# Kernel tuning notes

Hardware: AMD Instinct MI355X
Metric: run time of the kernel (lower is better)

Reference implementation:

```python
import jax, jax.numpy as jnp
import numpy as np

N = 100_000      # nodes
E = 1_600_000    # edges (avg degree 16)
H = 128          # hidden_channels == num_node_features
L = 6            # SAGEConv layers (third=True)
G = 128          # graphs in batch (for global_mean_pool)
C = 10           # num_classes
EPS = 1e-5       # BatchNorm eps


def setup_inputs() -> dict:
    key = jax.random.key(0)
    ks = jax.random.split(key, 8)
    s = 1.0 / np.sqrt(H)
    x = jax.random.normal(ks[0], (N, H), jnp.float32)
    edge_index = jax.random.randint(ks[1], (2, E), 0, N, dtype=jnp.int32)
    batch = jnp.sort(jax.random.randint(ks[2], (N,), 0, G, dtype=jnp.int32))
    return {
        "x": x,
        "edge_index": edge_index,
        "batch": batch,
        "Wl": jax.random.normal(ks[3], (L, H, H), jnp.float32) * s,  # neighbor lin
        "bl": jnp.zeros((L, H), jnp.float32),
        "Wr": jax.random.normal(ks[4], (L, H, H), jnp.float32) * s,  # root lin (no bias)
        "gamma": jnp.ones((L, H), jnp.float32),
        "beta": jnp.zeros((L, H), jnp.float32),
        "lin_W": jax.random.normal(ks[5], (H, C), jnp.float32) * s,
        "lin_b": jnp.zeros((C,), jnp.float32),
    }


def reference(x, edge_index, batch, Wl, bl, Wr, gamma, beta, lin_W, lin_b):
    src, dst = edge_index[0], edge_index[1]
    n = x.shape[0]
    # in-degree for mean aggregation (constant across layers)
    deg = jax.ops.segment_sum(jnp.ones((src.shape[0],), x.dtype), dst, num_segments=n)
    inv_deg = jnp.where(deg > 0, 1.0 / deg, 0.0)[:, None]  # [n,1]

    for l in range(Wl.shape[0]):
        # SAGEConv: lin_l(mean_{j->i} x_j) + lin_r(x_i)
        agg = jax.ops.segment_sum(x[src], dst, num_segments=n) * inv_deg  # [n,H]
        h = agg @ Wl[l] + bl[l] + x @ Wr[l]
        # BatchNorm1d (training-style batch stats, biased variance)
        mu = jnp.mean(h, axis=0)
        var = jnp.mean((h - mu) ** 2, axis=0)
        h = (h - mu) * jax.lax.rsqrt(var + EPS) * gamma[l] + beta[l]
        x = jax.nn.relu(h)

    # global_mean_pool over graph ids
    cnt = jax.ops.segment_sum(jnp.ones((n,), x.dtype), batch, num_segments=G)
    pooled = jax.ops.segment_sum(x, batch, num_segments=G) / jnp.maximum(cnt, 1.0)[:, None]
    # dropout(p=0.5) is identity in eval mode
    return pooled @ lin_W + lin_b  # [G, C]
```

## Files before the change

kernel.cpp:

```cpp
#include <hip/hip_runtime.h>
#include <hip/hip_bf16.h>

#define N_NODES 100000
#define N_EDGES 1600000
#define HDIM    128
#define NLAYER  6
#define NGRAPH  128
#define NCLASS  10
#define BN_EPS  1e-5f

#define POOL_SPLIT 16

#define NBUCK   196
#define BSH     9
#define KC_BLOCKS 250
#define KC_CHUNK  6400
#define LCOL_CAP  10240

#define GBM 128
#define NBLK_G ((N_NODES + GBM - 1) / GBM)

typedef __attribute__((ext_vector_type(8))) short short8v;
typedef __attribute__((ext_vector_type(4))) float f32x4;
typedef __attribute__((ext_vector_type(2))) float f32x2;
typedef __attribute__((ext_vector_type(4))) int int4v;
typedef __attribute__((ext_vector_type(2))) int int2v;

__device__ __forceinline__ float b2f(unsigned short h) {
    return __uint_as_float(((unsigned int)h) << 16);
}
__device__ __forceinline__ unsigned short f2b(float f) {
    unsigned int u = __float_as_uint(f);
    u += 0x7FFF + ((u >> 16) & 1);
    return (unsigned short)(u >> 16);
}
__device__ __forceinline__ void gl_lds16(const void* g, void* l) {
    __builtin_amdgcn_global_load_lds((const __attribute__((address_space(1))) unsigned int*)g,
                                     (__attribute__((address_space(3))) unsigned int*)l,
                                     16, 0, 0);
}
__device__ __forceinline__ short8v bn_pack(short8v v, float4 scA, float4 scB,
                                           float4 shA, float4 shB) {
    short8v o;
    o[0] = (short)f2b(fmaxf(0.f, b2f((unsigned short)v[0]) * scA.x + shA.x));
    o[1] = (short)f2b(fmaxf(0.f, b2f((unsigned short)v[1]) * scA.y + shA.y));
    o[2] = (short)f2b(fmaxf(0.f, b2f((unsigned short)v[2]) * scA.z + shA.z));
    o[3] = (short)f2b(fmaxf(0.f, b2f((unsigned short)v[3]) * scA.w + shA.w));
    o[4] = (short)f2b(fmaxf(0.f, b2f((unsigned short)v[4]) * scB.x + shB.x));
    o[5] = (short)f2b(fmaxf(0.f, b2f((unsigned short)v[5]) * scB.y + shB.y));
    o[6] = (short)f2b(fmaxf(0.f, b2f((unsigned short)v[6]) * scB.z + shB.z));
    o[7] = (short)f2b(fmaxf(0.f, b2f((unsigned short)v[7]) * scB.w + shB.w));
    return o;
}


__global__ void __launch_bounds__(256) k_hist(const int* __restrict__ dst,
                                              int* __restrict__ bcnt) {
    __shared__ int h[NBUCK];
    for (int i = threadIdx.x; i < NBUCK; i += 256) h[i] = 0;
    __syncthreads();
    const int4v* d4 = (const int4v*)dst;
    int base = blockIdx.x * (KC_CHUNK / 4);
    for (int i = threadIdx.x; i < KC_CHUNK / 4; i += 256) {
        int4v d = __builtin_nontemporal_load(d4 + base + i);
        atomicAdd(&h[d[0] >> BSH], 1);
        atomicAdd(&h[d[1] >> BSH], 1);
        atomicAdd(&h[d[2] >> BSH], 1);
        atomicAdd(&h[d[3] >> BSH], 1);
    }
    __syncthreads();
    for (int i = threadIdx.x; i < NBUCK; i += 256)
        if (h[i]) atomicAdd(&bcnt[i], h[i]);
}

__global__ void k_bscan(const int* __restrict__ bcnt, int* __restrict__ boff,
                        int* __restrict__ bcur, int* __restrict__ row_off) {
    if (threadIdx.x == 0 && blockIdx.x == 0) {
        int acc = 0;
        for (int i = 0; i < NBUCK; ++i) {
            boff[i] = acc; bcur[i] = acc; acc += bcnt[i];
        }
        boff[NBUCK] = acc;
        row_off[N_NODES] = N_EDGES;
    }
}

__global__ void __launch_bounds__(256) k_part(const int* __restrict__ src,
                                              const int* __restrict__ dst,
                                              int* __restrict__ bcur,
                                              int2v* __restrict__ P) {
    __shared__ int h[NBUCK];
    __shared__ int gbase[NBUCK];
    for (int i = threadIdx.x; i < NBUCK; i += 256) h[i] = 0;
    __syncthreads();
    const int4v* d4 = (const int4v*)dst;
    const int4v* s4 = (const int4v*)src;
    const int base = blockIdx.x * (KC_CHUNK / 4);
    for (int i = threadIdx.x; i < KC_CHUNK / 4; i += 256) {
        int4v d = __builtin_nontemporal_load(d4 + base + i);
        atomicAdd(&h[d[0] >> BSH], 1);
        atomicAdd(&h[d[1] >> BSH], 1);
        atomicAdd(&h[d[2] >> BSH], 1);
        atomicAdd(&h[d[3] >> BSH], 1);
    }
    __syncthreads();
    for (int i = threadIdx.x; i < NBUCK; i += 256) {
        int c = h[i];
        gbase[i] = c ? atomicAdd(&bcur[i], c) : 0;
        h[i] = 0;
    }
    __syncthreads();
    for (int i = threadIdx.x; i < KC_CHUNK / 4; i += 256) {
        int4v d = __builtin_nontemporal_load(d4 + base + i);
        int4v s = __builtin_nontemporal_load(s4 + base + i);
#pragma unroll
        for (int k = 0; k < 4; ++k) {
            int b = d[k] >> BSH;
            int pos = gbase[b] + atomicAdd(&h[b], 1);
            int2v pr; pr[0] = s[k]; pr[1] = d[k];
            P[pos] = pr;
        }
    }
}

__global__ void __launch_bounds__(1024) k_bucket(const int2v* __restrict__ P,
                                                 const int* __restrict__ boff,
                                                 int* __restrict__ row_off,
                                                 int* __restrict__ col) {
    __shared__ int ldeg[512];
    __shared__ int lcur[512];
    __shared__ int lcol[LCOL_CAP];
    const int tid = threadIdx.x;
    const int b = blockIdx.x;
    const int pbeg = boff[b], pend = boff[b + 1];
    const int nE = pend - pbeg;
    const int n0 = b << BSH;
    if (tid < 512) ldeg[tid] = 0;
    __syncthreads();
    for (int i = tid; i < nE; i += 1024) {
        int2v pr = P[pbeg + i];
        atomicAdd(&ldeg[pr[1] - n0], 1);
    }
    __syncthreads();
    int myd = (tid < 512) ? ldeg[tid] : 0;
    for (int off = 1; off < 512; off <<= 1) {
        int t = 0;
        if (tid < 512 && tid >= off) t = ldeg[tid - off];
        __syncthreads();
        if (tid < 512) ldeg[tid] += t;
        __syncthreads();
    }
    if (tid < 512) {
        int excl = ldeg[tid] - myd;
        lcur[tid] = excl;
        int node = n0 + tid;
        if (node < N_NODES) row_off[node] = pbeg + excl;
    }
    __syncthreads();
    for (int i = tid; i < nE; i += 1024) {
        int2v pr = P[pbeg + i];
        int pos = atomicAdd(&lcur[pr[1] - n0], 1);
        if (pos < LCOL_CAP) lcol[pos] = pr[0];
    }
    __syncthreads();
    for (int i = tid; i < nE; i += 1024) col[pbeg + i] = lcol[i];
}


__global__ void __launch_bounds__(256) k_cvt_x(const float* __restrict__ x,
                                               unsigned short* __restrict__ Xb,
                                               unsigned int* __restrict__ X8) {
    int idx = blockIdx.x * 256 + threadIdx.x;
    f32x4 v = __builtin_nontemporal_load(((const f32x4*)x) + idx);
    ushort4 o = { f2b(v[0]), f2b(v[1]), f2b(v[2]), f2b(v[3]) };
    ((ushort4*)Xb)[idx] = o;
    unsigned int d = 0;
    d = __builtin_amdgcn_cvt_pk_fp8_f32(v[0], v[1], d, false);
    d = __builtin_amdgcn_cvt_pk_fp8_f32(v[2], v[3], d, true);
    X8[idx] = d;
}

__global__ void __launch_bounds__(256) k_cvt_w(const float* __restrict__ Wl,
                                               const float* __restrict__ Wr,
                                               unsigned short* __restrict__ Wtb) {
    int idx = blockIdx.x * 256 + threadIdx.x;
    int kk = idx & 255;
    int n  = (idx >> 8) & 127;
    int l  = idx >> 15;
    float v = (kk < HDIM) ? Wl[l * HDIM * HDIM + kk * HDIM + n]
                          : Wr[l * HDIM * HDIM + (kk - HDIM) * HDIM + n];
    Wtb[idx] = f2b(v);
}

__global__ void __launch_bounds__(256) k_bnx8(const unsigned short* __restrict__ Hb,
                                              const float* __restrict__ scsh,
                                              int2v* __restrict__ X8) {
    int idx = blockIdx.x * 256 + threadIdx.x;
    int c8 = (idx & 15) * 8;
    short8v v = ((const short8v*)Hb)[idx];
    float f[8];
#pragma unroll
    for (int j = 0; j < 8; ++j)
        f[j] = fmaxf(0.f, b2f((unsigned short)v[j]) * scsh[c8 + j] + scsh[HDIM + c8 + j]);
    unsigned int d0 = 0, d1 = 0;
    d0 = __builtin_amdgcn_cvt_pk_fp8_f32(f[0], f[1], d0, false);
    d0 = __builtin_amdgcn_cvt_pk_fp8_f32(f[2], f[3], d0, true);
    d1 = __builtin_amdgcn_cvt_pk_fp8_f32(f[4], f[5], d1, false);
    d1 = __builtin_amdgcn_cvt_pk_fp8_f32(f[6], f[7], d1, true);
    int2v o; o[0] = (int)d0; o[1] = (int)d1;
    X8[idx] = o;
}


__global__ void __launch_bounds__(256) k_agg8(const unsigned char* __restrict__ X8,
                                              const int* __restrict__ row_off,
                                              const int* __restrict__ col,
                                              unsigned short* __restrict__ AGGb) {
    __shared__ int lcol[4096];
    __shared__ int sro[33];
    const int tid = threadIdx.x;
    const int nb0 = blockIdx.x * 32;
    if (tid <= 32) sro[tid] = row_off[nb0 + tid];
    __syncthreads();
    const int s0 = sro[0];
    const int nE = sro[32] - s0;
    const bool fits = (nE <= 4096);
    if (fits) {
        for (int i = tid; i < nE; i += 256) lcol[i] = col[s0 + i];
    }
    __syncthreads();

    const int g   = tid >> 3;
    const int c16 = (tid & 7) * 16;
    const int s = sro[g] - s0, e = sro[g + 1] - s0;
    const int* cp = fits ? lcol : (col + s0);

    f32x2 a2[8] = {};
    auto accum = [&](int4v v) {
#pragma unroll
        for (int q = 0; q < 4; ++q) {
            unsigned int w = (unsigned int)v[q];
            a2[2 * q]     += __builtin_amdgcn_cvt_pk_f32_fp8(w, false);
            a2[2 * q + 1] += __builtin_amdgcn_cvt_pk_f32_fp8(w, true);
        }
    };

    int p = s;
    for (; p + 8 <= e; p += 8) {
        int nbx[8];
#pragma unroll
        for (int j = 0; j < 8; ++j) nbx[j] = cp[p + j];
        int4v v[8];
#pragma unroll
        for (int j = 0; j < 8; ++j)
            v[j] = *(const int4v*)(X8 + (size_t)nbx[j] * HDIM + c16);
#pragma unroll
        for (int j = 0; j < 8; ++j) accum(v[j]);
    }
    if (p + 4 <= e) {
        int nbx[4];
#pragma unroll
        for (int j = 0; j < 4; ++j) nbx[j] = cp[p + j];
        int4v v[4];
#pragma unroll
        for (int j = 0; j < 4; ++j)
            v[j] = *(const int4v*)(X8 + (size_t)nbx[j] * HDIM + c16);
#pragma unroll
        for (int j = 0; j < 4; ++j) accum(v[j]);
        p += 4;
    }
    for (; p < e; ++p) {
        int4v v0 = *(const int4v*)(X8 + (size_t)cp[p] * HDIM + c16);
        accum(v0);
    }

    float w = (e > s) ? 1.0f / (float)(e - s) : 0.f;
    short8v o0, o1;
#pragma unroll
    for (int j = 0; j < 8; ++j) o0[j] = (short)f2b(a2[j >> 1][j & 1] * w);
#pragma unroll
    for (int j = 0; j < 8; ++j) o1[j] = (short)f2b(a2[4 + (j >> 1)][j & 1] * w);
    unsigned short* dst = AGGb + (size_t)(nb0 + g) * HDIM + c16;
    *(short8v*)dst = o0;
    *(short8v*)(dst + 8) = o1;
}


__global__ void __launch_bounds__(512) k_gemm_l0(const unsigned short* __restrict__ AGGb,
                                                 const unsigned short* __restrict__ Xb,
                                                 const unsigned short* __restrict__ Wtb,
                                                 const float* __restrict__ bl,
                                                 unsigned short* __restrict__ Hb,
                                                 float* __restrict__ pstat) {
    __shared__ __align__(16) char smem[32768];
    const int tid  = threadIdx.x;
    const int bm   = blockIdx.x * GBM;
    const int wv   = tid >> 6;
    const int lane = tid & 63;
    const int li   = lane & 15, hi = lane >> 4;
    const int wm   = wv & 1, wn = wv >> 1;

    f32x4 acc[4][2] = {};
    const int rr = tid >> 2, sk = tid & 3;
    const int swz = ((sk ^ (rr & 3)) << 4);

    auto stage = [&](int b, int step) {
        const unsigned short* Asrc = (step < 4) ? AGGb : Xb;
        const int kk0 = (step & 3) * 32;
        {
            int row = bm + rr; if (row >= N_NODES) row = N_NODES - 1;
            gl_lds16((const char*)(Asrc + (size_t)row * HDIM + kk0) + swz,
                     smem + b * 8192 + wv * 1024);
        }
        const int k0 = step * 32;
        gl_lds16((const char*)(Wtb + (size_t)rr * 256 + k0) + swz,
                 smem + 16384 + b * 8192 + wv * 1024);
    };

    stage(0, 0);
    __syncthreads();

    int buf = 0;
    for (int step = 0; step < 8; ++step) {
        if (step < 7) stage(buf ^ 1, step + 1);
        char* bA = smem + buf * 8192;
        char* bW = smem + 16384 + buf * 8192;
        short8v afr[4], bfr[2];
#pragma unroll
        for (int m = 0; m < 4; ++m) {
            int r = wm * 64 + m * 16 + li;
            afr[m] = *(const short8v*)(bA + r * 64 + ((hi ^ (r & 3)) << 4));
        }
#pragma unroll
        for (int nf = 0; nf < 2; ++nf) {
            int n = wn * 32 + nf * 16 + li;
            bfr[nf] = *(const short8v*)(bW + n * 64 + ((hi ^ (n & 3)) << 4));
        }
#pragma unroll
        for (int m = 0; m < 4; ++m)
#pragma unroll
            for (int nf = 0; nf < 2; ++nf)
                acc[m][nf] = __builtin_amdgcn_mfma_f32_16x16x32_bf16(afr[m], bfr[nf],
                                                                     acc[m][nf], 0, 0, 0);
        __syncthreads();
        buf ^= 1;
    }

    float* st = (float*)smem;
#pragma unroll
    for (int nf = 0; nf < 2; ++nf) {
        int c = wn * 32 + nf * 16 + li;
        float bb = bl[c];
        float ls = 0.f, lq = 0.f;
#pragma unroll
        for (int m = 0; m < 4; ++m) {
            int row0 = bm + wm * 64 + m * 16 + hi * 4;
#pragma unroll
            for (int j = 0; j < 4; ++j) {
                int row = row0 + j;
                if (row < N_NODES) {
                    float v = acc[m][nf][j] + bb;
                    Hb[(size_t)row * HDIM + c] = f2b(v);
                    ls += v; lq += v * v;
                }
            }
        }
        ls += __shfl_xor(ls, 16); ls += __shfl_xor(ls, 32);
        lq += __shfl_xor(lq, 16); lq += __shfl_xor(lq, 32);
        if (hi == 0) {
            st[wv * 128 + c] = ls;
            st[1024 + wv * 128 + c] = lq;
        }
    }
    __syncthreads();
    if (tid < 128) {
        int w0 = (tid >> 5) * 2;
        float s = st[w0 * 128 + tid] + st[(w0 + 1) * 128 + tid];
        pstat[blockIdx.x * 256 + tid] = s;
    } else if (tid < 256) {
        int c = tid - 128;
        int w0 = (c >> 5) * 2;
        float q = st[1024 + w0 * 128 + c] + st[1024 + (w0 + 1) * 128 + c];
        pstat[blockIdx.x * 256 + tid] = q;
    }
}

__global__ void __launch_bounds__(512) k_gemm_fuse(const unsigned short* __restrict__ AGGb,
                                                   const unsigned short* __restrict__ Hprev,
                                                   const float* __restrict__ scsh,
                                                   const unsigned short* __restrict__ Wtb,
                                                   const float* __restrict__ bl,
                                                   unsigned short* __restrict__ Hb,
                                                   float* __restrict__ pstat) {
    __shared__ __align__(16) char smem[32768];
    const int tid  = threadIdx.x;
    const int bm   = blockIdx.x * GBM;
    const int wv   = tid >> 6;
    const int lane = tid & 63;
    const int li   = lane & 15, hi = lane >> 4;
    const int wm   = wv & 1, wn = wv >> 1;

    f32x4 acc[4][2] = {};
    const int rr = tid >> 2, sk = tid & 3;
    const int swz = ((sk ^ (rr & 3)) << 4);

    auto stageW = [&](int b, int step) {
        const int k0 = step * 32;
        gl_lds16((const char*)(Wtb + (size_t)rr * 256 + k0) + swz,
                 smem + 16384 + b * 8192 + wv * 1024);
    };
    auto stageA = [&](int b, int step) {
        const int kk0 = step * 32;
        int row = bm + rr; if (row >= N_NODES) row = N_NODES - 1;
        gl_lds16((const char*)(AGGb + (size_t)row * HDIM + kk0) + swz,
                 smem + b * 8192 + wv * 1024);
    };

    stageA(0, 0); stageW(0, 0);
    __syncthreads();

    int buf = 0;
    for (int step = 0; step < 8; ++step) {
        char* curA = smem + buf * 8192;
        char* curW = smem + 16384 + buf * 8192;
        char* nxtA = smem + (buf ^ 1) * 8192;
        const int ns = step + 1;
        short8v rv;
        int c0 = 0;
        bool regstage = false;
        if (step < 7) {
            stageW(buf ^ 1, ns);
            if (ns < 4) {
                stageA(buf ^ 1, ns);
            } else {
                regstage = true;
                c0 = (ns - 4) * 32 + sk * 8;
                int row = bm + rr; if (row >= N_NODES) row = N_NODES - 1;
                rv = *(const short8v*)(Hprev + (size_t)row * HDIM + c0);
            }
        }

        short8v afr[4], bfr[2];
#pragma unroll
        for (int m = 0; m < 4; ++m) {
            int r = wm * 64 + m * 16 + li;
            afr[m] = *(const short8v*)(curA + r * 64 + ((hi ^ (r & 3)) << 4));
        }
#pragma unroll
        for (int nf = 0; nf < 2; ++nf) {
            int n = wn * 32 + nf * 16 + li;
            bfr[nf] = *(const short8v*)(curW + n * 64 + ((hi ^ (n & 3)) << 4));
        }
#pragma unroll
        for (int m = 0; m < 4; ++m)
#pragma unroll
            for (int nf = 0; nf < 2; ++nf)
                acc[m][nf] = __builtin_amdgcn_mfma_f32_16x16x32_bf16(afr[m], bfr[nf],
                                                                     acc[m][nf], 0, 0, 0);

        if (regstage) {
            float4 scA = *(const float4*)&scsh[c0];
            float4 scB = *(const float4*)&scsh[c0 + 4];
            float4 shA = *(const float4*)&scsh[HDIM + c0];
            float4 shB = *(const float4*)&scsh[HDIM + c0 + 4];
            *(short8v*)(nxtA + rr * 64 + swz) = bn_pack(rv, scA, scB, shA, shB);
        }
        __syncthreads();
        buf ^= 1;
    }

    float* st = (float*)smem;
#pragma unroll
    for (int nf = 0; nf < 2; ++nf) {
        int c = wn * 32 + nf * 16 + li;
        float bb = bl[c];
        float ls = 0.f, lq = 0.f;
#pragma unroll
        for (int m = 0; m < 4; ++m) {
            int row0 = bm + wm * 64 + m * 16 + hi * 4;
#pragma unroll
            for (int j = 0; j < 4; ++j) {
                int row = row0 + j;
                if (row < N_NODES) {
                    float v = acc[m][nf][j] + bb;
                    Hb[(size_t)row * HDIM + c] = f2b(v);
                    ls += v; lq += v * v;
                }
            }
        }
        ls += __shfl_xor(ls, 16); ls += __shfl_xor(ls, 32);
        lq += __shfl_xor(lq, 16); lq += __shfl_xor(lq, 32);
        if (hi == 0) {
            st[wv * 128 + c] = ls;
            st[1024 + wv * 128 + c] = lq;
        }
    }
    __syncthreads();
    if (tid < 128) {
        int w0 = (tid >> 5) * 2;
        float s = st[w0 * 128 + tid] + st[(w0 + 1) * 128 + tid];
        pstat[blockIdx.x * 256 + tid] = s;
    } else if (tid < 256) {
        int c = tid - 128;
        int w0 = (c >> 5) * 2;
        float q = st[1024 + w0 * 128 + c] + st[1024 + (w0 + 1) * 128 + c];
        pstat[blockIdx.x * 256 + tid] = q;
    }
}

__global__ void __launch_bounds__(256) k_red1(const float* __restrict__ pstat,
                                              float* __restrict__ red32) {
    int c = threadIdx.x, b = blockIdx.x;
    float s = 0.f;
    for (int r = b; r < NBLK_G; r += 32) s += pstat[r * 256 + c];
    red32[b * 256 + c] = s;
}

__global__ void __launch_bounds__(128) k_stats_final(const float* __restrict__ red32,
                                                     const float* __restrict__ gamma,
                                                     const float* __restrict__ beta,
                                                     float* __restrict__ scsh) {
    int c = threadIdx.x;
    float s = 0.f, q = 0.f;
    for (int r = 0; r < 32; ++r) { s += red32[r * 256 + c]; q += red32[r * 256 + 128 + c]; }
    float mu = s / (float)N_NODES;
    float var = q / (float)N_NODES - mu * mu;
    float rs = rsqrtf(var + BN_EPS);
    float sc = gamma[c] * rs;
    scsh[c] = sc;
    scsh[HDIM + c] = beta[c] - mu * sc;
}


__global__ void k_gbound(const int* __restrict__ batch, int* __restrict__ gb) {
    int t = blockIdx.x * 64 + threadIdx.x;
    if (t > NGRAPH) return;
    int lo = 0, hi = N_NODES;
    while (lo < hi) { int mid = (lo + hi) >> 1; if (batch[mid] < t) lo = mid + 1; else hi = mid; }
    gb[t] = lo;
}

__global__ void __launch_bounds__(128) k_pool_part(const unsigned short* __restrict__ Hb,
                                                   const float* __restrict__ scsh,
                                                   const int* __restrict__ gb,
                                                   float* __restrict__ ppart) {
    int g = blockIdx.x, sp = blockIdx.y;
    int c = threadIdx.x;
    float sc = scsh[c], sh = scsh[HDIM + c];
    int s = gb[g], e = gb[g + 1];
    float acc = 0.f;
    for (int i = s + sp; i < e; i += POOL_SPLIT)
        acc += fmaxf(0.f, b2f(Hb[(size_t)i * HDIM + c]) * sc + sh);
    ppart[(g * POOL_SPLIT + sp) * HDIM + c] = acc;
}

__global__ void __launch_bounds__(128) k_pool_final(const int* __restrict__ gb,
                                                    const float* __restrict__ ppart,
                                                    float* __restrict__ pooled) {
    int g = blockIdx.x, c = threadIdx.x;
    float s = 0.f;
    for (int sp = 0; sp < POOL_SPLIT; ++sp) s += ppart[(g * POOL_SPLIT + sp) * HDIM + c];
    int cnt = gb[g + 1] - gb[g]; if (cnt < 1) cnt = 1;
    pooled[g * HDIM + c] = s / (float)cnt;
}

__global__ void __launch_bounds__(128) k_lin(const float* __restrict__ pooled,
                                             const float* __restrict__ W,
                                             const float* __restrict__ bvec,
                                             float* __restrict__ out) {
    __shared__ float p[HDIM];
    int g = blockIdx.x, t = threadIdx.x;
    p[t] = pooled[g * HDIM + t];
    __syncthreads();
    if (t < NCLASS) {
        float acc = bvec[t];
        for (int k = 0; k < HDIM; ++k) acc += p[k] * W[k * NCLASS + t];
        out[g * NCLASS + t] = acc;
    }
}


extern "C" void kernel_launch(void* const* d_in, const int* in_sizes, int n_in,
                              void* d_out, int out_size, void* d_ws, size_t ws_size,
                              hipStream_t stream) {
    const float* x     = (const float*)d_in[0];
    const int*   eidx  = (const int*)d_in[1];
    const int*   batch = (const int*)d_in[2];
    const float* Wl    = (const float*)d_in[3];
    const float* bl    = (const float*)d_in[4];
    const float* Wr    = (const float*)d_in[5];
    const float* gamma = (const float*)d_in[6];
    const float* beta  = (const float*)d_in[7];
    const float* linW  = (const float*)d_in[8];
    const float* linb  = (const float*)d_in[9];
    float* out = (float*)d_out;

    const int* src = eidx;
    const int* dst = eidx + N_EDGES;

    char* p = (char*)d_ws;
    auto alloc = [&](size_t bytes) { char* r = p; p += (bytes + 255) & ~(size_t)255; return r; };
    unsigned short* Xb   = (unsigned short*)alloc((size_t)N_NODES * HDIM * 2);
    unsigned char*  X8   = (unsigned char*)alloc((size_t)N_NODES * HDIM);
    unsigned short* AGGb = (unsigned short*)alloc((size_t)N_NODES * HDIM * 2);
    unsigned short* HbA  = (unsigned short*)alloc((size_t)N_NODES * HDIM * 2);
    unsigned short* HbB  = (unsigned short*)alloc((size_t)N_NODES * HDIM * 2);
    unsigned short* Wtb  = (unsigned short*)alloc((size_t)NLAYER * 2 * HDIM * HDIM * 2);
    int*   row_off = (int*)alloc((N_NODES + 2) * 4);
    int*   col     = (int*)alloc((size_t)N_EDGES * 4);
    int2v* P       = (int2v*)alloc((size_t)N_EDGES * 8);
    int*   bcnt    = (int*)alloc(NBUCK * 4);
    int*   boff    = (int*)alloc((NBUCK + 1) * 4);
    int*   bcur    = (int*)alloc(NBUCK * 4);
    int*   gb      = (int*)alloc((NGRAPH + 2) * 4);
    float* pstat   = (float*)alloc((size_t)NBLK_G * 256 * 4);
    float* red32   = (float*)alloc(32 * 256 * 4);
    float* scsh    = (float*)alloc(2 * HDIM * 4);
    float* ppart   = (float*)alloc((size_t)NGRAPH * POOL_SPLIT * HDIM * 4);
    float* pooled  = (float*)alloc(NGRAPH * HDIM * 4);

    hipMemsetAsync(bcnt, 0, NBUCK * sizeof(int), stream);
    k_hist<<<KC_BLOCKS, 256, 0, stream>>>(dst, bcnt);
    k_bscan<<<1, 64, 0, stream>>>(bcnt, boff, bcur, row_off);
    k_part<<<KC_BLOCKS, 256, 0, stream>>>(src, dst, bcur, P);
    k_bucket<<<NBUCK, 1024, 0, stream>>>(P, boff, row_off, col);

    k_cvt_x<<<N_NODES * HDIM / 4 / 256, 256, 0, stream>>>(x, Xb, (unsigned int*)X8);
    k_cvt_w<<<NLAYER * 2 * HDIM * HDIM / 256, 256, 0, stream>>>(Wl, Wr, Wtb);
    k_gbound<<<3, 64, 0, stream>>>(batch, gb);

    k_agg8<<<N_NODES / 32, 256, 0, stream>>>(X8, row_off, col, AGGb);
    k_gemm_l0<<<NBLK_G, 512, 0, stream>>>(AGGb, Xb, Wtb, bl, HbA, pstat);
    k_red1<<<32, 256, 0, stream>>>(pstat, red32);
    k_stats_final<<<1, 128, 0, stream>>>(red32, gamma, beta, scsh);

    unsigned short* Hcur = HbA;
    for (int l = 1; l < NLAYER; ++l) {
        unsigned short* Hout = (l & 1) ? HbB : HbA;
        k_bnx8<<<N_NODES * HDIM / 8 / 256, 256, 0, stream>>>(Hcur, scsh, (int2v*)X8);
        k_agg8<<<N_NODES / 32, 256, 0, stream>>>(X8, row_off, col, AGGb);
        k_gemm_fuse<<<NBLK_G, 512, 0, stream>>>(
            AGGb, Hcur, scsh, Wtb + (size_t)l * 2 * HDIM * HDIM, bl + (size_t)l * HDIM,
            Hout, pstat);
        k_red1<<<32, 256, 0, stream>>>(pstat, red32);
        k_stats_final<<<1, 128, 0, stream>>>(red32, gamma + (size_t)l * HDIM,
                                             beta + (size_t)l * HDIM, scsh);
        Hcur = Hout;
    }

    k_pool_part<<<dim3(NGRAPH, POOL_SPLIT), 128, 0, stream>>>(Hcur, scsh, gb, ppart);
    k_pool_final<<<NGRAPH, 128, 0, stream>>>(gb, ppart, pooled);
    k_lin<<<NGRAPH, 128, 0, stream>>>(pooled, linW, linb, out);
}
```

Measured before the change: 562.5 us.

## Fuse BatchNorm stats reduction into GEMM via last-block atomic counter

Removes the separate k_red1 and k_stats_final launches after each GEMM. Each GEMM block writes its partial column sums, then increments an atomic counter, and the last block to finish reduces all partials and computes the BN scale and shift. Per-layer scale/shift buffers replace the single shared one, so the next layer's read does not race with the write. This saves two launches per layer in exchange for a serial tail of reduction work done by one block.

Result: slower. 1.481 ms (+163.3%).

```diff
diff --git a/kernel.cpp b/kernel.cpp
--- a/kernel.cpp
+++ b/kernel.cpp
@@ -285,13 +285,54 @@
     *(short8v*)(dst + 8) = o1;
 }
 
+__device__ __forceinline__ void stats_tail(char* smem, const float* __restrict__ pstat,
+                                           int* __restrict__ done,
+                                           const float* __restrict__ gamma,
+                                           const float* __restrict__ beta,
+                                           float* __restrict__ scshOut, int tid) {
+    __threadfence();
+    __shared__ int lastFlag;
+    if (tid == 0) lastFlag = (atomicAdd(done, 1) == NBLK_G - 1) ? 1 : 0;
+    __syncthreads();
+    if (!lastFlag) return;
+    __threadfence();
+    float* smemF = (float*)smem;
+    const int q = tid & 63, half = tid >> 6;
+    f32x4 part = {0.f, 0.f, 0.f, 0.f};
+    for (int r = half; r < NBLK_G; r += 8)
+        part += *(const f32x4*)(pstat + r * 256 + q * 4);
+    ((f32x4*)smemF)[half * 64 + q] = part;
+    __syncthreads();
+    if (tid < 64) {
+        f32x4 s = ((const f32x4*)smemF)[tid];
+#pragma unroll
+        for (int h = 1; h < 8; ++h) s += ((const f32x4*)smemF)[h * 64 + tid];
+        *(f32x4*)(smemF + 2048 + tid * 4) = s;
+    }
+    __syncthreads();
+    if (tid < 128) {
+        float ssum = smemF[2048 + tid];
+        float ssq  = smemF[2048 + 128 + tid];
+        float mu = ssum / (float)N_NODES;
+        float var = ssq / (float)N_NODES - mu * mu;
+        float rs = rsqrtf(var + BN_EPS);
+        float sc = gamma[tid] * rs;
+        scshOut[tid] = sc;
+        scshOut[HDIM + tid] = beta[tid] - mu * sc;
+    }
+}
+
 
 __global__ void __launch_bounds__(512) k_gemm_l0(const unsigned short* __restrict__ AGGb,
                                                  const unsigned short* __restrict__ Xb,
                                                  const unsigned short* __restrict__ Wtb,
                                                  const float* __restrict__ bl,
                                                  unsigned short* __restrict__ Hb,
-                                                 float* __restrict__ pstat) {
+                                                 float* __restrict__ pstat,
+                                                 int* __restrict__ done,
+                                                 const float* __restrict__ gamma,
+                                                 const float* __restrict__ beta,
+                                                 float* __restrict__ scshOut) {
     __shared__ __align__(16) char smem[32768];
     const int tid  = threadIdx.x;
     const int bm   = blockIdx.x * GBM;
@@ -383,6 +424,8 @@
         float q = st[1024 + w0 * 128 + c] + st[1024 + (w0 + 1) * 128 + c];
         pstat[blockIdx.x * 256 + tid] = q;
     }
+    __syncthreads();
+    stats_tail(smem, pstat, done, gamma, beta, scshOut, tid);
 }
 
 __global__ void __launch_bounds__(512) k_gemm_fuse(const unsigned short* __restrict__ AGGb,
@@ -391,7 +434,11 @@
                                                    const unsigned short* __restrict__ Wtb,
                                                    const float* __restrict__ bl,
                                                    unsigned short* __restrict__ Hb,
-                                                   float* __restrict__ pstat) {
+                                                   float* __restrict__ pstat,
+                                                   int* __restrict__ done,
+                                                   const float* __restrict__ gamma,
+                                                   const float* __restrict__ beta,
+                                                   float* __restrict__ scshOut) {
     __shared__ __align__(16) char smem[32768];
     const int tid  = threadIdx.x;
     const int bm   = blockIdx.x * GBM;
@@ -506,29 +553,8 @@
         float q = st[1024 + w0 * 128 + c] + st[1024 + (w0 + 1) * 128 + c];
         pstat[blockIdx.x * 256 + tid] = q;
     }
-}
-
-__global__ void __launch_bounds__(256) k_red1(const float* __restrict__ pstat,
-                                              float* __restrict__ red32) {
-    int c = threadIdx.x, b = blockIdx.x;
-    float s = 0.f;
-    for (int r = b; r < NBLK_G; r += 32) s += pstat[r * 256 + c];
-    red32[b * 256 + c] = s;
-}
-
-__global__ void __launch_bounds__(128) k_stats_final(const float* __restrict__ red32,
-                                                     const float* __restrict__ gamma,
-                                                     const float* __restrict__ beta,
-                                                     float* __restrict__ scsh) {
-    int c = threadIdx.x;
-    float s = 0.f, q = 0.f;
-    for (int r = 0; r < 32; ++r) { s += red32[r * 256 + c]; q += red32[r * 256 + 128 + c]; }
-    float mu = s / (float)N_NODES;
-    float var = q / (float)N_NODES - mu * mu;
-    float rs = rsqrtf(var + BN_EPS);
-    float sc = gamma[c] * rs;
-    scsh[c] = sc;
-    scsh[HDIM + c] = beta[c] - mu * sc;
+    __syncthreads();
+    stats_tail(smem, pstat, done, gamma, beta, scshOut, tid);
 }
 
 
@@ -612,14 +638,15 @@
     int*   bcnt    = (int*)alloc(NBUCK * 4);
     int*   boff    = (int*)alloc((NBUCK + 1) * 4);
     int*   bcur    = (int*)alloc(NBUCK * 4);
+    int*   done    = (int*)alloc(8 * 4);
     int*   gb      = (int*)alloc((NGRAPH + 2) * 4);
     float* pstat   = (float*)alloc((size_t)NBLK_G * 256 * 4);
-    float* red32   = (float*)alloc(32 * 256 * 4);
-    float* scsh    = (float*)alloc(2 * HDIM * 4);
+    float* scshAll = (float*)alloc((size_t)NLAYER * 256 * 4);
     float* ppart   = (float*)alloc((size_t)NGRAPH * POOL_SPLIT * HDIM * 4);
     float* pooled  = (float*)alloc(NGRAPH * HDIM * 4);
 
     hipMemsetAsync(bcnt, 0, NBUCK * sizeof(int), stream);
+    hipMemsetAsync(done, 0, 8 * sizeof(int), stream);
     k_hist<<<KC_BLOCKS, 256, 0, stream>>>(dst, bcnt);
     k_bscan<<<1, 64, 0, stream>>>(bcnt, boff, bcur, row_off);
     k_part<<<KC_BLOCKS, 256, 0, stream>>>(src, dst, bcur, P);
@@ -630,25 +657,25 @@
     k_gbound<<<3, 64, 0, stream>>>(batch, gb);
 
     k_agg8<<<N_NODES / 32, 256, 0, stream>>>(X8, row_off, col, AGGb);
-    k_gemm_l0<<<NBLK_G, 512, 0, stream>>>(AGGb, Xb, Wtb, bl, HbA, pstat);
-    k_red1<<<32, 256, 0, stream>>>(pstat, red32);
-    k_stats_final<<<1, 128, 0, stream>>>(red32, gamma, beta, scsh);
+    k_gemm_l0<<<NBLK_G, 512, 0, stream>>>(AGGb, Xb, Wtb, bl, HbA, pstat,
+                                          done + 0, gamma, beta, scshAll);
 
     unsigned short* Hcur = HbA;
     for (int l = 1; l < NLAYER; ++l) {
         unsigned short* Hout = (l & 1) ? HbB : HbA;
-        k_bnx8<<<N_NODES * HDIM / 8 / 256, 256, 0, stream>>>(Hcur, scsh, (int2v*)X8);
+        const float* scshPrev = scshAll + (size_t)(l - 1) * 256;
+        float* scshCur        = scshAll + (size_t)l * 256;
+        k_bnx8<<<N_NODES * HDIM / 8 / 256, 256, 0, stream>>>(Hcur, scshPrev, (int2v*)X8);
         k_agg8<<<N_NODES / 32, 256, 0, stream>>>(X8, row_off, col, AGGb);
         k_gemm_fuse<<<NBLK_G, 512, 0, stream>>>(
-            AGGb, Hcur, scsh, Wtb + (size_t)l * 2 * HDIM * HDIM, bl + (size_t)l * HDIM,
-            Hout, pstat);
-        k_red1<<<32, 256, 0, stream>>>(pstat, red32);
-        k_stats_final<<<1, 128, 0, stream>>>(red32, gamma + (size_t)l * HDIM,
-                                             beta + (size_t)l * HDIM, scsh);
+            AGGb, Hcur, scshPrev, Wtb + (size_t)l * 2 * HDIM * HDIM, bl + (size_t)l * HDIM,
+            Hout, pstat, done + l, gamma + (size_t)l * HDIM, beta + (size_t)l * HDIM,
+            scshCur);
         Hcur = Hout;
     }
 
-    k_pool_part<<<dim3(NGRAPH, POOL_SPLIT), 128, 0, stream>>>(Hcur, scsh, gb, ppart);
+    k_pool_part<<<dim3(NGRAPH, POOL_SPLIT), 128, 0, stream>>>(
+        Hcur, scshAll + (size_t)(NLAYER - 1) * 256, gb, ppart);
     k_pool_final<<<NGRAPH, 128, 0, stream>>>(gb, ppart, pooled);
     k_lin<<<NGRAPH, 128, 0, stream>>>(pooled, linW, linb, out);
 }
```
